# Kernel optimization log

Hardware: AMD Instinct MI355X
Metric: run time of the kernel (lower is better)

The kernel has to match this reference:

```python
import jax, jax.numpy as jnp
import numpy as np

BATCH = 8192
IN_F = 4096
OUT_F = 4096


def setup_inputs() -> dict:
    key = jax.random.key(0)
    k_x, k_w, k_m = jax.random.split(key, 3)
    x = jax.random.normal(k_x, (BATCH, IN_F), dtype=jnp.float32)
    # kaiming_normal_ for relu: std = sqrt(2 / fan_in) with fan_in = in_features
    std = float(np.sqrt(2.0 / IN_F))
    weight = jax.random.normal(k_w, (OUT_F, IN_F), dtype=jnp.float32) * std
    bias = jnp.zeros((OUT_F,), dtype=jnp.float32)
    mask = jax.random.bernoulli(k_m, 0.5, (OUT_F, IN_F)).astype(jnp.float32)
    return {"x": x, "weight": weight, "bias": bias, "mask": mask}


def reference(x, weight, bias, mask):
    # masked_weight = weight * mask; out = x @ masked_weight.T + bias
    masked_weight = weight * mask                      # [out, in]
    return jnp.einsum("bi,oi->bo", x, masked_weight) + bias  # [batch, out]
```

## Files before the change

kernel.cpp:

```cpp
#include <hip/hip_runtime.h>
#include <hip/hip_bf16.h>
#include <stdint.h>

#define BATCH 8192
#define IN_F  4096
#define OUT_F 4096

#define BM 128
#define BN 128
#define BK 64

typedef __attribute__((ext_vector_type(8)))  short bf16x8;
typedef __attribute__((ext_vector_type(16))) float f32x16;


__device__ __forceinline__ unsigned short f2bf(float f) {
    unsigned int u = __float_as_uint(f);
    unsigned int lsb = (u >> 16) & 1u;
    u += 0x7fffu + lsb;
    return (unsigned short)(u >> 16);
}

__device__ __forceinline__ void gl_lds16(const void* g, void* l) {
    __builtin_amdgcn_global_load_lds(
        (const __attribute__((address_space(1))) void*)g,
        (__attribute__((address_space(3))) void*)l,
        16, 0, 0);
}

#define XBLK ((BATCH * IN_F) / 8 / 256)
#define WBLK ((OUT_F * IN_F) / 8 / 256)

__global__ __launch_bounds__(256) void cvt_kernel(const float4* __restrict__ x,
                                                  const float4* __restrict__ w,
                                                  const float4* __restrict__ m,
                                                  uint4* __restrict__ xo,
                                                  uint4* __restrict__ wo) {
    int b = blockIdx.x;
    union { unsigned short u[8]; uint4 v; } r;
    if (b < XBLK) {
        int i = b * 256 + threadIdx.x;
        float4 a0 = x[2 * i], a1 = x[2 * i + 1];
        r.u[0] = f2bf(a0.x); r.u[1] = f2bf(a0.y); r.u[2] = f2bf(a0.z); r.u[3] = f2bf(a0.w);
        r.u[4] = f2bf(a1.x); r.u[5] = f2bf(a1.y); r.u[6] = f2bf(a1.z); r.u[7] = f2bf(a1.w);
        xo[i] = r.v;
    } else {
        int i = (b - XBLK) * 256 + threadIdx.x;
        float4 wa = w[2 * i], wb = w[2 * i + 1];
        float4 ma = m[2 * i], mb = m[2 * i + 1];
        r.u[0] = f2bf(wa.x * ma.x); r.u[1] = f2bf(wa.y * ma.y);
        r.u[2] = f2bf(wa.z * ma.z); r.u[3] = f2bf(wa.w * ma.w);
        r.u[4] = f2bf(wb.x * mb.x); r.u[5] = f2bf(wb.y * mb.y);
        r.u[6] = f2bf(wb.z * mb.z); r.u[7] = f2bf(wb.w * mb.w);
        wo[i] = r.v;
    }
}

__global__ __launch_bounds__(256, 4) void gemm_kernel(const unsigned short* __restrict__ A,
                                                      const unsigned short* __restrict__ W,
                                                      const float* __restrict__ bias,
                                                      float* __restrict__ C) {
    __shared__ unsigned short lA[BM * BK];
    __shared__ unsigned short lB[BN * BK];

    const int tid  = threadIdx.x;
    const int lane = tid & 63;
    const int wave = tid >> 6;
    const int bm = blockIdx.y;
    const int bn = blockIdx.x;

    const int wm = (wave & 1) * 64;
    const int wn = (wave >> 1) * 64;
    const int r32 = lane & 31;
    const int hi  = lane >> 5;
    const int swz = lane & 7;

    f32x16 acc[2][2] = {};

    const unsigned short* Ab = A + (size_t)(bm * BM) * IN_F;
    const unsigned short* Wb = W + (size_t)(bn * BN) * IN_F;

    int rowS[4], cgS[4], ldsoff[4];
#pragma unroll
    for (int i = 0; i < 4; ++i) {
        int s = i * 256 + tid;
        rowS[i] = s >> 3;
        cgS[i]  = (s & 7) ^ (rowS[i] & 7);
        ldsoff[i] = s * 8;
    }

    for (int kt = 0; kt < IN_F; kt += BK) {
#pragma unroll
        for (int i = 0; i < 4; ++i) {
            gl_lds16(Ab + (size_t)rowS[i] * IN_F + kt + cgS[i] * 8, &lA[ldsoff[i]]);
            gl_lds16(Wb + (size_t)rowS[i] * IN_F + kt + cgS[i] * 8, &lB[ldsoff[i]]);
        }
        __syncthreads();

#pragma unroll
        for (int ks = 0; ks < 4; ++ks) {
            const int c = ((ks * 2 + hi) ^ swz) * 8;
            bf16x8 af[2], bfj[2];
#pragma unroll
            for (int i = 0; i < 2; ++i)
                af[i] = *(const bf16x8*)&lA[(wm + i * 32 + r32) * BK + c];
#pragma unroll
            for (int j = 0; j < 2; ++j)
                bfj[j] = *(const bf16x8*)&lB[(wn + j * 32 + r32) * BK + c];
#pragma unroll
            for (int i = 0; i < 2; ++i)
#pragma unroll
                for (int j = 0; j < 2; ++j)
                    acc[i][j] = __builtin_amdgcn_mfma_f32_32x32x16_bf16(
                        af[i], bfj[j], acc[i][j], 0, 0, 0);
        }
        __syncthreads();
    }

    const int crow0 = bm * BM + wm;
    const int ccol0 = bn * BN + wn;
#pragma unroll
    for (int j = 0; j < 2; ++j) {
        const int col = ccol0 + j * 32 + r32;
        const float bj = bias[col];
#pragma unroll
        for (int i = 0; i < 2; ++i) {
#pragma unroll
            for (int reg = 0; reg < 16; ++reg) {
                int row = crow0 + i * 32 + (reg & 3) + 8 * (reg >> 2) + 4 * hi;
                C[(size_t)row * OUT_F + col] = acc[i][j][reg] + bj;
            }
        }
    }
}

__global__ __launch_bounds__(256) void fallback_kernel(const float* __restrict__ x,
                                                       const float* __restrict__ w,
                                                       const float* __restrict__ bias,
                                                       const float* __restrict__ m,
                                                       float* __restrict__ out) {
    size_t idx = (size_t)blockIdx.x * 256 + threadIdx.x;
    int row = (int)(idx >> 12);
    int col = (int)(idx & (OUT_F - 1));
    const float4* xr = (const float4*)(x + (size_t)row * IN_F);
    const float4* wr = (const float4*)(w + (size_t)col * IN_F);
    const float4* mr = (const float4*)(m + (size_t)col * IN_F);
    float s = 0.f;
    for (int k = 0; k < IN_F / 4; ++k) {
        float4 xv = xr[k], wv = wr[k], mv = mr[k];
        s += xv.x * wv.x * mv.x + xv.y * wv.y * mv.y +
             xv.z * wv.z * mv.z + xv.w * wv.w * mv.w;
    }
    out[idx] = s + bias[col];
}


extern "C" void kernel_launch(void* const* d_in, const int* in_sizes, int n_in,
                              void* d_out, int out_size, void* d_ws, size_t ws_size,
                              hipStream_t stream) {
    const float* x    = (const float*)d_in[0];
    const float* w    = (const float*)d_in[1];
    const float* bias = (const float*)d_in[2];
    const float* mask = (const float*)d_in[3];
    float* out = (float*)d_out;

    const size_t need = ((size_t)BATCH * IN_F + (size_t)OUT_F * IN_F) * sizeof(unsigned short);
    if (ws_size < need) {
        fallback_kernel<<<(size_t)BATCH * OUT_F / 256, 256, 0, stream>>>(
            x, w, bias, mask, out);
        return;
    }

    unsigned short* xb = (unsigned short*)d_ws;
    unsigned short* wb = xb + (size_t)BATCH * IN_F;

    cvt_kernel<<<XBLK + WBLK, 256, 0, stream>>>(
        (const float4*)x, (const float4*)w, (const float4*)mask,
        (uint4*)xb, (uint4*)wb);

    dim3 grid(OUT_F / BN, BATCH / BM);
    gemm_kernel<<<grid, 256, 0, stream>>>(xb, wb, bias, out);
}
```

Before: 590.1 us.

## Use two waves per block with 64x128 warp tiles and new LDS swizzle

```diff
diff --git a/kernel.cpp b/kernel.cpp
--- a/kernel.cpp
+++ b/kernel.cpp
@@ -9,6 +9,7 @@
 #define BM 128
 #define BN 128
 #define BK 64
+#define THREADS 128
 
 typedef __attribute__((ext_vector_type(8)))  short bf16x8;
 typedef __attribute__((ext_vector_type(16))) float f32x16;
@@ -26,6 +27,10 @@
         (const __attribute__((address_space(1))) void*)g,
         (__attribute__((address_space(3))) void*)l,
         16, 0, 0);
+}
+
+__device__ __forceinline__ int sigma(int row) {
+    return (row ^ (row >> 3)) & 7;
 }
 
 #define XBLK ((BATCH * IN_F) / 8 / 256)
@@ -56,10 +61,10 @@
     }
 }
 
-__global__ __launch_bounds__(256, 4) void gemm_kernel(const unsigned short* __restrict__ A,
-                                                      const unsigned short* __restrict__ W,
-                                                      const float* __restrict__ bias,
-                                                      float* __restrict__ C) {
+__global__ __launch_bounds__(THREADS, 2) void gemm_kernel(const unsigned short* __restrict__ A,
+                                                          const unsigned short* __restrict__ W,
+                                                          const float* __restrict__ bias,
+                                                          float* __restrict__ C) {
     __shared__ unsigned short lA[BM * BK];
     __shared__ unsigned short lB[BN * BK];
 
@@ -69,48 +74,60 @@
     const int bm = blockIdx.y;
     const int bn = blockIdx.x;
 
-    const int wm = (wave & 1) * 64;
-    const int wn = (wave >> 1) * 64;
+    const int wm  = wave * 64;
     const int r32 = lane & 31;
     const int hi  = lane >> 5;
-    const int swz = lane & 7;
-
-    f32x16 acc[2][2] = {};
+
+    f32x16 acc[2][4] = {};
 
     const unsigned short* Ab = A + (size_t)(bm * BM) * IN_F;
     const unsigned short* Wb = W + (size_t)(bn * BN) * IN_F;
 
-    int rowS[4], cgS[4], ldsoff[4];
-#pragma unroll
-    for (int i = 0; i < 4; ++i) {
-        int s = i * 256 + tid;
-        rowS[i] = s >> 3;
-        cgS[i]  = (s & 7) ^ (rowS[i] & 7);
-        ldsoff[i] = s * 8;
+    int goff[8], loff[8];
+#pragma unroll
+    for (int i = 0; i < 8; ++i) {
+        int s = i * THREADS + tid;
+        int row = s >> 3;
+        int g = (s & 7) ^ sigma(row);
+        goff[i] = row * IN_F + g * 8;
+        loff[i] = s * 8;
+    }
+
+    int aoff[2], asig[2], boff[4], bsig[4];
+#pragma unroll
+    for (int i = 0; i < 2; ++i) {
+        int row = wm + i * 32 + r32;
+        aoff[i] = row * BK; asig[i] = sigma(row);
+    }
+#pragma unroll
+    for (int j = 0; j < 4; ++j) {
+        int row = j * 32 + r32;
+        boff[j] = row * BK; bsig[j] = sigma(row);
     }
 
     for (int kt = 0; kt < IN_F; kt += BK) {
 #pragma unroll
-        for (int i = 0; i < 4; ++i) {
-            gl_lds16(Ab + (size_t)rowS[i] * IN_F + kt + cgS[i] * 8, &lA[ldsoff[i]]);
-            gl_lds16(Wb + (size_t)rowS[i] * IN_F + kt + cgS[i] * 8, &lB[ldsoff[i]]);
-        }
+        for (int i = 0; i < 8; ++i)
+            gl_lds16(Ab + goff[i] + kt, &lA[loff[i]]);
+#pragma unroll
+        for (int i = 0; i < 8; ++i)
+            gl_lds16(Wb + goff[i] + kt, &lB[loff[i]]);
         __syncthreads();
 
 #pragma unroll
         for (int ks = 0; ks < 4; ++ks) {
-            const int c = ((ks * 2 + hi) ^ swz) * 8;
-            bf16x8 af[2], bfj[2];
+            const int g = ks * 2 + hi;
+            bf16x8 af[2], bfj[4];
 #pragma unroll
             for (int i = 0; i < 2; ++i)
-                af[i] = *(const bf16x8*)&lA[(wm + i * 32 + r32) * BK + c];
-#pragma unroll
-            for (int j = 0; j < 2; ++j)
-                bfj[j] = *(const bf16x8*)&lB[(wn + j * 32 + r32) * BK + c];
-#pragma unroll
-            for (int i = 0; i < 2; ++i)
-#pragma unroll
-                for (int j = 0; j < 2; ++j)
+                af[i] = *(const bf16x8*)&lA[aoff[i] + ((g ^ asig[i]) << 3)];
+#pragma unroll
+            for (int j = 0; j < 4; ++j)
+                bfj[j] = *(const bf16x8*)&lB[boff[j] + ((g ^ bsig[j]) << 3)];
+#pragma unroll
+            for (int j = 0; j < 4; ++j)
+#pragma unroll
+                for (int i = 0; i < 2; ++i)
                     acc[i][j] = __builtin_amdgcn_mfma_f32_32x32x16_bf16(
                         af[i], bfj[j], acc[i][j], 0, 0, 0);
         }
@@ -118,9 +135,9 @@
     }
 
     const int crow0 = bm * BM + wm;
-    const int ccol0 = bn * BN + wn;
-#pragma unroll
-    for (int j = 0; j < 2; ++j) {
+    const int ccol0 = bn * BN;
+#pragma unroll
+    for (int j = 0; j < 4; ++j) {
         const int col = ccol0 + j * 32 + r32;
         const float bj = bias[col];
 #pragma unroll
@@ -179,5 +196,5 @@
         (uint4*)xb, (uint4*)wb);
 
     dim3 grid(OUT_F / BN, BATCH / BM);
-    gemm_kernel<<<grid, 256, 0, stream>>>(xb, wb, bias, out);
-}
+    gemm_kernel<<<grid, THREADS, 0, stream>>>(xb, wb, bias, out);
+}
```

Measured after the change: 595.8 us. About the same (+1.0%).
